# Performance work log

Hardware: AMD Instinct MI355X
Metric: run time of the kernel (lower is better)

Reference implementation:

```python
import jax, jax.numpy as jnp
import numpy as np


def setup_inputs() -> dict:
    key = jax.random.key(0)
    k1, k2 = jax.random.split(key)
    B, S, D_IN, D_OUT = 4, 8192, 768, 768
    x = jax.random.normal(k1, (B, S, D_IN), dtype=jnp.float32)
    # kaiming_normal_(mode='fan_out', nonlinearity='linear') -> std = 1/sqrt(fan_out)
    weight = jax.random.normal(k2, (D_OUT, D_IN), dtype=jnp.float32) * (1.0 / jnp.sqrt(D_OUT))
    return {"x": x, "weight": weight}


def reference(x, weight):
    # Binarize weights with sign (0 -> 0, matching torch.sign), then F.linear:
    # out[..., o] = sum_i x[..., i] * sign(W)[o, i]
    w_bin = jnp.sign(weight)
    return jnp.einsum('bsi,oi->bso', x, w_bin)
```

## Files before the change

kernel.cpp:

```cpp
#include <hip/hip_runtime.h>
#include <hip/hip_bf16.h>

using f32x4 = __attribute__((ext_vector_type(4))) float;
using s16x8 = __attribute__((ext_vector_type(8))) short;

constexpr int KDIM = 768;
constexpr int NDIM = 768;
constexpr int BM = 128;
constexpr int BN = 128;
constexpr int BK = 32;
constexpr int KLD = BK + 8;
constexpr int NT = KDIM / BK;

__device__ __forceinline__ short f2bf(float f) {
    unsigned u = __builtin_bit_cast(unsigned, f);
    u += 0x7FFFu + ((u >> 16) & 1u);
    return (short)(unsigned short)(u >> 16);
}

__device__ __forceinline__ short sgnbf(float w) {
    return w > 0.f ? (short)(unsigned short)0x3F80u
                   : (w < 0.f ? (short)(unsigned short)0xBF80u : (short)0);
}

__device__ __forceinline__ s16x8 cvt8(float4 u, float4 v) {
    s16x8 r;
    r[0] = f2bf(u.x); r[1] = f2bf(u.y); r[2] = f2bf(u.z); r[3] = f2bf(u.w);
    r[4] = f2bf(v.x); r[5] = f2bf(v.y); r[6] = f2bf(v.z); r[7] = f2bf(v.w);
    return r;
}

__device__ __forceinline__ s16x8 sgn8(float4 u, float4 v) {
    s16x8 r;
    r[0] = sgnbf(u.x); r[1] = sgnbf(u.y); r[2] = sgnbf(u.z); r[3] = sgnbf(u.w);
    r[4] = sgnbf(v.x); r[5] = sgnbf(v.y); r[6] = sgnbf(v.z); r[7] = sgnbf(v.w);
    return r;
}

__global__ __launch_bounds__(256, 2)
void binlin_mfma(const float* __restrict__ X, const float* __restrict__ W,
                 float* __restrict__ Out, int M) {
    __shared__ __align__(16) unsigned short As[2][BM][KLD];
    __shared__ __align__(16) unsigned short Bs[2][BN][KLD];

    const int nbn = NDIM / BN;
    const int nwg = gridDim.x;
    const int bid = blockIdx.x;
    const int cpx = nwg >> 3;
    const int swz = (bid & 7) * cpx + (bid >> 3);
    const int bm = swz / nbn;
    const int bn = swz - bm * nbn;

    const int t    = threadIdx.x;
    const int lane = t & 63;
    const int wid  = t >> 6;
    const int wm   = (wid >> 1) * 64;
    const int wn   = (wid & 1) * 64;
    const int lr   = lane & 15;
    const int lk   = (lane >> 4) * 8;

    const float* Xb = X + (size_t)bm * BM * KDIM;
    const float* Wb = W + (size_t)bn * BN * KDIM;

    const int r0 = t >> 2;
    const int c0 = (t & 3) * 8;

    f32x4 acc[4][4] = {};

    {
        const float* xa  = Xb + (size_t)r0 * KDIM + c0;
        const float* xa2 = xa + (size_t)64 * KDIM;
        float4 a0 = *(const float4*)xa;
        float4 a1 = *(const float4*)(xa + 4);
        float4 a2 = *(const float4*)xa2;
        float4 a3 = *(const float4*)(xa2 + 4);
        const float* wa  = Wb + (size_t)r0 * KDIM + c0;
        const float* wa2 = wa + (size_t)64 * KDIM;
        float4 b0 = *(const float4*)wa;
        float4 b1 = *(const float4*)(wa + 4);
        float4 b2 = *(const float4*)wa2;
        float4 b3 = *(const float4*)(wa2 + 4);

        *(s16x8*)&As[0][r0][c0]      = cvt8(a0, a1);
        *(s16x8*)&As[0][r0 + 64][c0] = cvt8(a2, a3);
        *(s16x8*)&Bs[0][r0][c0]      = sgn8(b0, b1);
        *(s16x8*)&Bs[0][r0 + 64][c0] = sgn8(b2, b3);
    }
    __syncthreads();

    for (int kt = 0; kt < NT; ++kt) {
        const int buf = kt & 1;
        const bool pf = (kt + 1 < NT);

        float4 a0, a1, a2, a3, b0, b1, b2, b3;
        if (pf) {
            const float* xa  = Xb + (size_t)r0 * KDIM + (kt + 1) * BK + c0;
            const float* xa2 = xa + (size_t)64 * KDIM;
            a0 = *(const float4*)xa;
            a1 = *(const float4*)(xa + 4);
            a2 = *(const float4*)xa2;
            a3 = *(const float4*)(xa2 + 4);
            const float* wa  = Wb + (size_t)r0 * KDIM + (kt + 1) * BK + c0;
            const float* wa2 = wa + (size_t)64 * KDIM;
            b0 = *(const float4*)wa;
            b1 = *(const float4*)(wa + 4);
            b2 = *(const float4*)wa2;
            b3 = *(const float4*)(wa2 + 4);
        }

        s16x8 af[4], bfr[4];
        #pragma unroll
        for (int m = 0; m < 4; ++m)
            af[m] = *(const s16x8*)&As[buf][wm + m * 16 + lr][lk];
        #pragma unroll
        for (int n = 0; n < 4; ++n)
            bfr[n] = *(const s16x8*)&Bs[buf][wn + n * 16 + lr][lk];
        #pragma unroll
        for (int m = 0; m < 4; ++m)
            #pragma unroll
            for (int n = 0; n < 4; ++n)
                acc[m][n] = __builtin_amdgcn_mfma_f32_16x16x32_bf16(
                    af[m], bfr[n], acc[m][n], 0, 0, 0);

        if (pf) {
            const int nb = buf ^ 1;
            *(s16x8*)&As[nb][r0][c0]      = cvt8(a0, a1);
            *(s16x8*)&As[nb][r0 + 64][c0] = cvt8(a2, a3);
            *(s16x8*)&Bs[nb][r0][c0]      = sgn8(b0, b1);
            *(s16x8*)&Bs[nb][r0 + 64][c0] = sgn8(b2, b3);
        }
        __syncthreads();
    }

    float* Ob = Out + (size_t)(bm * BM) * NDIM + bn * BN;
    #pragma unroll
    for (int m = 0; m < 4; ++m) {
        const int row0 = wm + m * 16 + (lane >> 4) * 4;
        #pragma unroll
        for (int n = 0; n < 4; ++n) {
            const int col = wn + n * 16 + lr;
            #pragma unroll
            for (int r = 0; r < 4; ++r)
                Ob[(size_t)(row0 + r) * NDIM + col] = acc[m][n][r];
        }
    }
}

extern "C" void kernel_launch(void* const* d_in, const int* in_sizes, int n_in,
                              void* d_out, int out_size, void* d_ws, size_t ws_size,
                              hipStream_t stream) {
    const float* X = (const float*)d_in[0];
    const float* W = (const float*)d_in[1];
    float* Out = (float*)d_out;
    const int M = in_sizes[0] / KDIM;
    const int grid = (M / BM) * (NDIM / BN);
    binlin_mfma<<<grid, 256, 0, stream>>>(X, W, Out, M);
}
```

Baseline: 74.86 us.

## Pre-binarize weights into MFMA fragment layout and read B directly from global

Adds a small pre-pass kernel that binarizes the weight matrix into bf16 laid out in MFMA fragment order in the workspace. The main GEMM then loads B fragments straight from global/L2 with one 16-byte load per fragment instead of staging them in LDS, which removes the B shared-memory tile and its per-block sign conversion. BK is doubled to 64 to halve the number of barriers, and the bf16 conversion uses the built-in cast. The cost is an extra kernel launch, and every wave now issues global loads for B inside the MFMA loop, which may add latency there.

```diff
diff --git a/kernel.cpp b/kernel.cpp
--- a/kernel.cpp
+++ b/kernel.cpp
@@ -8,45 +8,46 @@
 constexpr int NDIM = 768;
 constexpr int BM = 128;
 constexpr int BN = 128;
-constexpr int BK = 32;
+constexpr int BK = 64;
 constexpr int KLD = BK + 8;
-constexpr int NT = KDIM / BK;
+constexpr int NT2 = KDIM / BK;
+constexpr int NKT = KDIM / 32;
+constexpr int N16 = NDIM / 16;
 
-__device__ __forceinline__ short f2bf(float f) {
-    unsigned u = __builtin_bit_cast(unsigned, f);
-    u += 0x7FFFu + ((u >> 16) & 1u);
-    return (short)(unsigned short)(u >> 16);
+__device__ __forceinline__ unsigned short f2bf(float f) {
+    __bf16 h = (__bf16)f;
+    return __builtin_bit_cast(unsigned short, h);
 }
 
-__device__ __forceinline__ short sgnbf(float w) {
-    return w > 0.f ? (short)(unsigned short)0x3F80u
-                   : (w < 0.f ? (short)(unsigned short)0xBF80u : (short)0);
+__global__ void binarize_w(const float* __restrict__ W, unsigned short* __restrict__ Wf) {
+    const int g = blockIdx.x * 256 + threadIdx.x;
+    const int lane = g & 63;
+    const int grp  = g >> 6;
+    const int kt   = grp % NKT;
+    const int n16  = grp / NKT;
+    const int col  = n16 * 16 + (lane & 15);
+    const int k0   = kt * 32 + (lane >> 4) * 8;
+    const float* src = W + (size_t)col * KDIM + k0;
+    s16x8 r;
+    #pragma unroll
+    for (int j = 0; j < 8; ++j) {
+        float w = src[j];
+        unsigned u = __builtin_bit_cast(unsigned, w);
+        r[j] = (w != 0.f) ? (short)(unsigned short)(0x3F80u | ((u >> 16) & 0x8000u))
+                          : (short)0;
+    }
+    *(s16x8*)(Wf + (size_t)g * 8) = r;
 }
 
-__device__ __forceinline__ s16x8 cvt8(float4 u, float4 v) {
-    s16x8 r;
-    r[0] = f2bf(u.x); r[1] = f2bf(u.y); r[2] = f2bf(u.z); r[3] = f2bf(u.w);
-    r[4] = f2bf(v.x); r[5] = f2bf(v.y); r[6] = f2bf(v.z); r[7] = f2bf(v.w);
-    return r;
-}
-
-__device__ __forceinline__ s16x8 sgn8(float4 u, float4 v) {
-    s16x8 r;
-    r[0] = sgnbf(u.x); r[1] = sgnbf(u.y); r[2] = sgnbf(u.z); r[3] = sgnbf(u.w);
-    r[4] = sgnbf(v.x); r[5] = sgnbf(v.y); r[6] = sgnbf(v.z); r[7] = sgnbf(v.w);
-    return r;
-}
-
+template<bool PRE>
 __global__ __launch_bounds__(256, 2)
 void binlin_mfma(const float* __restrict__ X, const float* __restrict__ W,
-                 float* __restrict__ Out, int M) {
+                 const unsigned short* __restrict__ Wf, float* __restrict__ Out) {
     __shared__ __align__(16) unsigned short As[2][BM][KLD];
-    __shared__ __align__(16) unsigned short Bs[2][BN][KLD];
 
     const int nbn = NDIM / BN;
-    const int nwg = gridDim.x;
     const int bid = blockIdx.x;
-    const int cpx = nwg >> 3;
+    const int cpx = gridDim.x >> 3;
     const int swz = (bid & 7) * cpx + (bid >> 3);
     const int bm = swz / nbn;
     const int bn = swz - bm * nbn;
@@ -60,74 +61,93 @@
     const int lk   = (lane >> 4) * 8;
 
     const float* Xb = X + (size_t)bm * BM * KDIM;
-    const float* Wb = W + (size_t)bn * BN * KDIM;
-
-    const int r0 = t >> 2;
-    const int c0 = (t & 3) * 8;
+    const int srow = t >> 1;
+    const int scol = (t & 1) * 32;
 
     f32x4 acc[4][4] = {};
 
     {
-        const float* xa  = Xb + (size_t)r0 * KDIM + c0;
-        const float* xa2 = xa + (size_t)64 * KDIM;
-        float4 a0 = *(const float4*)xa;
-        float4 a1 = *(const float4*)(xa + 4);
-        float4 a2 = *(const float4*)xa2;
-        float4 a3 = *(const float4*)(xa2 + 4);
-        const float* wa  = Wb + (size_t)r0 * KDIM + c0;
-        const float* wa2 = wa + (size_t)64 * KDIM;
-        float4 b0 = *(const float4*)wa;
-        float4 b1 = *(const float4*)(wa + 4);
-        float4 b2 = *(const float4*)wa2;
-        float4 b3 = *(const float4*)(wa2 + 4);
-
-        *(s16x8*)&As[0][r0][c0]      = cvt8(a0, a1);
-        *(s16x8*)&As[0][r0 + 64][c0] = cvt8(a2, a3);
-        *(s16x8*)&Bs[0][r0][c0]      = sgn8(b0, b1);
-        *(s16x8*)&Bs[0][r0 + 64][c0] = sgn8(b2, b3);
+        const float* p = Xb + (size_t)srow * KDIM + scol;
+        float4 a[8];
+        #pragma unroll
+        for (int i = 0; i < 8; ++i) a[i] = *(const float4*)(p + i * 4);
+        #pragma unroll
+        for (int i = 0; i < 4; ++i) {
+            s16x8 c;
+            c[0] = (short)f2bf(a[2*i].x);   c[1] = (short)f2bf(a[2*i].y);
+            c[2] = (short)f2bf(a[2*i].z);   c[3] = (short)f2bf(a[2*i].w);
+            c[4] = (short)f2bf(a[2*i+1].x); c[5] = (short)f2bf(a[2*i+1].y);
+            c[6] = (short)f2bf(a[2*i+1].z); c[7] = (short)f2bf(a[2*i+1].w);
+            *(s16x8*)&As[0][srow][scol + i * 8] = c;
+        }
     }
     __syncthreads();
 
-    for (int kt = 0; kt < NT; ++kt) {
+    const int fb = bn * 8 + (wn >> 4);
+
+    for (int kt = 0; kt < NT2; ++kt) {
         const int buf = kt & 1;
-        const bool pf = (kt + 1 < NT);
+        const bool pf = (kt + 1 < NT2);
 
-        float4 a0, a1, a2, a3, b0, b1, b2, b3;
+        float4 a[8];
         if (pf) {
-            const float* xa  = Xb + (size_t)r0 * KDIM + (kt + 1) * BK + c0;
-            const float* xa2 = xa + (size_t)64 * KDIM;
-            a0 = *(const float4*)xa;
-            a1 = *(const float4*)(xa + 4);
-            a2 = *(const float4*)xa2;
-            a3 = *(const float4*)(xa2 + 4);
-            const float* wa  = Wb + (size_t)r0 * KDIM + (kt + 1) * BK + c0;
-            const float* wa2 = wa + (size_t)64 * KDIM;
-            b0 = *(const float4*)wa;
-            b1 = *(const float4*)(wa + 4);
-            b2 = *(const float4*)wa2;
-            b3 = *(const float4*)(wa2 + 4);
+            const float* p = Xb + (size_t)srow * KDIM + (kt + 1) * BK + scol;
+            #pragma unroll
+            for (int i = 0; i < 8; ++i) a[i] = *(const float4*)(p + i * 4);
         }
 
-        s16x8 af[4], bfr[4];
+        s16x8 bf_[2][4];
         #pragma unroll
-        for (int m = 0; m < 4; ++m)
-            af[m] = *(const s16x8*)&As[buf][wm + m * 16 + lr][lk];
+        for (int kk = 0; kk < 2; ++kk)
+            #pragma unroll
+            for (int n = 0; n < 4; ++n) {
+                if (PRE) {
+                    const size_t idx = ((size_t)((fb + n) * NKT + (kt * 2 + kk)) * 64 + lane) * 8;
+                    bf_[kk][n] = *(const s16x8*)(Wf + idx);
+                } else {
+                    const int col = bn * BN + wn + n * 16 + lr;
+                    const int k0  = (kt * 2 + kk) * 32 + lk;
+                    const float* wp = W + (size_t)col * KDIM + k0;
+                    float4 w0 = *(const float4*)wp, w1 = *(const float4*)(wp + 4);
+                    float ww[8] = {w0.x, w0.y, w0.z, w0.w, w1.x, w1.y, w1.z, w1.w};
+                    s16x8 r;
+                    #pragma unroll
+                    for (int j = 0; j < 8; ++j) {
+                        unsigned u = __builtin_bit_cast(unsigned, ww[j]);
+                        r[j] = (ww[j] != 0.f) ? (short)(unsigned short)(0x3F80u | ((u >> 16) & 0x8000u))
+                                              : (short)0;
+                    }
+                    bf_[kk][n] = r;
+                }
+            }
+
+        s16x8 af[2][4];
         #pragma unroll
-        for (int n = 0; n < 4; ++n)
-            bfr[n] = *(const s16x8*)&Bs[buf][wn + n * 16 + lr][lk];
+        for (int kk = 0; kk < 2; ++kk)
+            #pragma unroll
+            for (int m = 0; m < 4; ++m)
+                af[kk][m] = *(const s16x8*)&As[buf][wm + m * 16 + lr][kk * 32 + lk];
+
         #pragma unroll
-        for (int m = 0; m < 4; ++m)
+        for (int kk = 0; kk < 2; ++kk)
             #pragma unroll
-            for (int n = 0; n < 4; ++n)
-                acc[m][n] = __builtin_amdgcn_mfma_f32_16x16x32_bf16(
-                    af[m], bfr[n], acc[m][n], 0, 0, 0);
+            for (int m = 0; m < 4; ++m)
+                #pragma unroll
+                for (int n = 0; n < 4; ++n)
+                    acc[m][n] = __builtin_amdgcn_mfma_f32_16x16x32_bf16(
+                        af[kk][m], bf_[kk][n], acc[m][n], 0, 0, 0);
 
         if (pf) {
             const int nb = buf ^ 1;
-            *(s16x8*)&As[nb][r0][c0]      = cvt8(a0, a1);
-            *(s16x8*)&As[nb][r0 + 64][c0] = cvt8(a2, a3);
-            *(s16x8*)&Bs[nb][r0][c0]      = sgn8(b0, b1);
-            *(s16x8*)&Bs[nb][r0 + 64][c0] = sgn8(b2, b3);
+            #pragma unroll
+            for (int i = 0; i < 4; ++i) {
+                s16x8 c;
+                c[0] = (short)f2bf(a[2*i].x);   c[1] = (short)f2bf(a[2*i].y);
+                c[2] = (short)f2bf(a[2*i].z);   c[3] = (short)f2bf(a[2*i].w);
+                c[4] = (short)f2bf(a[2*i+1].x); c[5] = (short)f2bf(a[2*i+1].y);
+                c[6] = (short)f2bf(a[2*i+1].z); c[7] = (short)f2bf(a[2*i+1].w);
+                *(s16x8*)&As[nb][srow][scol + i * 8] = c;
+            }
         }
         __syncthreads();
     }
@@ -154,5 +174,13 @@
     float* Out = (float*)d_out;
     const int M = in_sizes[0] / KDIM;
     const int grid = (M / BM) * (NDIM / BN);
-    binlin_mfma<<<grid, 256, 0, stream>>>(X, W, Out, M);
+    const size_t need = (size_t)NDIM * KDIM * sizeof(unsigned short);
+
+    if (ws_size >= need) {
+        unsigned short* Wf = (unsigned short*)d_ws;
+        binarize_w<<<(N16 * NKT * 64) / 256, 256, 0, stream>>>(W, Wf);
+        binlin_mfma<true><<<grid, 256, 0, stream>>>(X, W, Wf, Out);
+    } else {
+        binlin_mfma<false><<<grid, 256, 0, stream>>>(X, W, nullptr, Out);
+    }
 }
```

Result: slower. 120.6 us (+61.1%).
